# Optimization experiments

Hardware: AMD Instinct MI355X
Metric: run time of the kernel (lower is better)

## Reference

```python
import jax, jax.numpy as jnp
import numpy as np

N_QUERIES = 16384
N_TRAIN = 16384


def setup_inputs() -> dict:
    key = jax.random.key(0)
    k1, k2, k3 = jax.random.split(key, 3)
    queries = jax.random.normal(k1, (N_QUERIES,), dtype=jnp.float32)
    x_train = jax.random.normal(k2, (N_TRAIN,), dtype=jnp.float32)
    y_train = jax.random.normal(k3, (N_TRAIN,), dtype=jnp.float32)
    w = jnp.ones((N_TRAIN,), dtype=jnp.float32)  # learned bandwidth param
    return {"queries": queries, "x_train": x_train, "y_train": y_train, "w": w}


def reference(queries, x_train, y_train, w):
    # pairwise diff: [n_q, n_train]
    diff = queries[:, None] - x_train[None, :]
    scores = -jnp.square(diff * w) * 0.5
    attn = jax.nn.softmax(scores, axis=1)  # [n_q, n_train]
    return attn @ y_train  # [n_q]
```

## Files before the change

### kernel.cpp

```cpp
#include <hip/hip_runtime.h>

#if defined(__has_builtin)
#if __has_builtin(__builtin_amdgcn_exp2f)
#define EXP2F(x) __builtin_amdgcn_exp2f(x)
#endif
#endif
#ifndef EXP2F
#define EXP2F(x) exp2f(x)
#endif

#define BLOCK 256
#define QPT 8
#define TILE 512
#define MAX_SEGS 128
#define RSPLIT 4

typedef float v2f __attribute__((ext_vector_type(2)));

#define KFOLD 0.8493218f

__global__ __launch_bounds__(BLOCK) void nw_partial(
    const float* __restrict__ q, const float* __restrict__ xt,
    const float* __restrict__ yt, const float* __restrict__ w,
    float2* __restrict__ partial, int n_q, int n_t, int segs)
{
    __shared__ float4 tile[TILE];
    const int seg = blockIdx.x;
    const int tid = threadIdx.x;
    const int qbase = blockIdx.y * (BLOCK * QPT) + tid;

    v2f q2[QPT / 2];
    v2f acc[QPT];
#pragma unroll
    for (int i = 0; i < QPT; ++i) {
        int qi = qbase + i * BLOCK;
        float qv = (qi < n_q) ? q[qi] : 0.f;
        if (i & 1) q2[i >> 1].y = qv; else q2[i >> 1].x = qv;
        acc[i] = (v2f){0.f, 0.f};
    }

    const int seg_len = (n_t + segs - 1) / segs;
    const int s0 = seg * seg_len;
    const int s1 = min(s0 + seg_len, n_t);

    for (int base = s0; base < s1; base += TILE) {
        const int cnt = min(TILE, s1 - base);
        __syncthreads();
        for (int j = tid; j < cnt; j += BLOCK) {
            float a = w[base + j] * KFOLD;
            tile[j] = make_float4(a, -xt[base + j] * a, yt[base + j], 0.f);
        }
        __syncthreads();
#pragma unroll 2
        for (int j = 0; j < cnt; ++j) {
            float4 v = tile[j];
            v2f a2  = (v2f){v.x, v.x};
            v2f nb2 = (v2f){v.y, v.y};
            v2f ym  = (v2f){v.z, 1.0f};
#pragma unroll
            for (int p = 0; p < QPT / 2; ++p) {
                v2f t = __builtin_elementwise_fma(q2[p], a2, nb2);
                v2f s = -(t * t);
                float e0 = EXP2F(s.x);
                float e1 = EXP2F(s.y);
                acc[2 * p]     = __builtin_elementwise_fma((v2f){e0, e0}, ym,
                                                           acc[2 * p]);
                acc[2 * p + 1] = __builtin_elementwise_fma((v2f){e1, e1}, ym,
                                                           acc[2 * p + 1]);
            }
        }
    }

#pragma unroll
    for (int i = 0; i < QPT; ++i) {
        int qi = qbase + i * BLOCK;
        if (qi < n_q) partial[seg * n_q + qi] = make_float2(acc[i].x, acc[i].y);
    }
}

__global__ __launch_bounds__(BLOCK) void nw_reduce(
    const float2* __restrict__ partial, float* __restrict__ out,
    int n_q, int segs)
{
    __shared__ float2 red[RSPLIT][64];
    const int tid = threadIdx.x;
    const int c = tid >> 6;
    const int ql = tid & 63;
    const int qi = blockIdx.x * 64 + ql;

    float num = 0.f, den = 0.f;
    if (qi < n_q) {
        for (int s = c; s < segs; s += RSPLIT) {
            float2 p = partial[(size_t)s * n_q + qi];
            num += p.x;
            den += p.y;
        }
    }
    red[c][ql] = make_float2(num, den);
    __syncthreads();
    if (c == 0 && qi < n_q) {
        float2 r1 = red[1][ql], r2 = red[2][ql], r3 = red[3][ql];
        num += r1.x + r2.x + r3.x;
        den += r1.y + r2.y + r3.y;
        out[qi] = num / den;
    }
}

extern "C" void kernel_launch(void* const* d_in, const int* in_sizes, int n_in,
                              void* d_out, int out_size, void* d_ws, size_t ws_size,
                              hipStream_t stream) {
    const float* q  = (const float*)d_in[0];
    const float* xt = (const float*)d_in[1];
    const float* yt = (const float*)d_in[2];
    const float* w  = (const float*)d_in[3];
    const int n_q = in_sizes[0];
    const int n_t = in_sizes[1];

    int segs = MAX_SEGS;
    size_t need = (size_t)segs * (size_t)n_q * sizeof(float2);
    if (need > ws_size) {
        segs = (int)(ws_size / ((size_t)n_q * sizeof(float2)));
        if (segs < 1) segs = 1;
    }

    float2* partial = (float2*)d_ws;
    dim3 grid(segs, (n_q + BLOCK * QPT - 1) / (BLOCK * QPT));
    nw_partial<<<grid, BLOCK, 0, stream>>>(q, xt, yt, w, partial, n_q, n_t, segs);
    nw_reduce<<<(n_q + 63) / 64, BLOCK, 0, stream>>>(partial, (float*)d_out,
                                                     n_q, segs);
}
```

Before: 107.4 us.

## Pair train points per query and accumulate with packed fp16 dot products

Restructures the inner loop so each query processes two training points at once with packed FMAs. The two exponentials are packed to fp16 and accumulated into numerator and denominator with fdot2 against fp16 y values and ones. The shared tile is split into a float4 of scale/bias pairs plus packed half y values, and the segment count doubles to raise parallelism. It aims to cut VALU instructions per pair, but fp16 rounding of the weights and y values loses accuracy, and more segments add reduce traffic.

```diff
diff --git a/kernel.cpp b/kernel.cpp
--- a/kernel.cpp
+++ b/kernel.cpp
@@ -3,6 +3,9 @@
 #if defined(__has_builtin)
 #if __has_builtin(__builtin_amdgcn_exp2f)
 #define EXP2F(x) __builtin_amdgcn_exp2f(x)
+#endif
+#if __has_builtin(__builtin_amdgcn_fdot2)
+#define HAVE_FDOT2 1
 #endif
 #endif
 #ifndef EXP2F
@@ -12,10 +15,12 @@
 #define BLOCK 256
 #define QPT 8
 #define TILE 512
-#define MAX_SEGS 128
+#define TILE2 (TILE / 2)
+#define MAX_SEGS 256
 #define RSPLIT 4
 
 typedef float v2f __attribute__((ext_vector_type(2)));
+typedef _Float16 h2 __attribute__((ext_vector_type(2)));
 
 #define KFOLD 0.8493218f
 
@@ -24,49 +29,74 @@
     const float* __restrict__ yt, const float* __restrict__ w,
     float2* __restrict__ partial, int n_q, int n_t, int segs)
 {
-    __shared__ float4 tile[TILE];
+    __shared__ float4 tileA[TILE2];
+    __shared__ unsigned int tileY[TILE2];
+
     const int seg = blockIdx.x;
     const int tid = threadIdx.x;
     const int qbase = blockIdx.y * (BLOCK * QPT) + tid;
 
-    v2f q2[QPT / 2];
-    v2f acc[QPT];
+    v2f q2[QPT];
+    float num[QPT], den[QPT];
 #pragma unroll
     for (int i = 0; i < QPT; ++i) {
         int qi = qbase + i * BLOCK;
         float qv = (qi < n_q) ? q[qi] : 0.f;
-        if (i & 1) q2[i >> 1].y = qv; else q2[i >> 1].x = qv;
-        acc[i] = (v2f){0.f, 0.f};
+        q2[i] = (v2f){qv, qv};
+        num[i] = 0.f;
+        den[i] = 0.f;
     }
 
     const int seg_len = (n_t + segs - 1) / segs;
     const int s0 = seg * seg_len;
     const int s1 = min(s0 + seg_len, n_t);
 
+    const h2 one2 = {(_Float16)1.0f, (_Float16)1.0f};
+
     for (int base = s0; base < s1; base += TILE) {
         const int cnt = min(TILE, s1 - base);
+        const int cnt2 = (cnt + 1) >> 1;
         __syncthreads();
-        for (int j = tid; j < cnt; j += BLOCK) {
-            float a = w[base + j] * KFOLD;
-            tile[j] = make_float4(a, -xt[base + j] * a, yt[base + j], 0.f);
+        for (int j2 = tid; j2 < cnt2; j2 += BLOCK) {
+            int j0 = base + 2 * j2;
+            int j1 = j0 + 1;
+            float a0 = w[j0] * KFOLD;
+            float nb0 = -xt[j0] * a0;
+            float y0 = yt[j0];
+            float a1 = 0.f, nb1 = 1.0e4f, y1 = 0.f;
+            if (j1 < s1) {
+                a1 = w[j1] * KFOLD;
+                nb1 = -xt[j1] * a1;
+                y1 = yt[j1];
+            }
+            tileA[j2] = make_float4(a0, a1, nb0, nb1);
+            h2 yh = {(_Float16)y0, (_Float16)y1};
+            tileY[j2] = __builtin_bit_cast(unsigned int, yh);
         }
         __syncthreads();
 #pragma unroll 2
-        for (int j = 0; j < cnt; ++j) {
-            float4 v = tile[j];
-            v2f a2  = (v2f){v.x, v.x};
-            v2f nb2 = (v2f){v.y, v.y};
-            v2f ym  = (v2f){v.z, 1.0f};
+        for (int j2 = 0; j2 < cnt2; ++j2) {
+            float4 A = tileA[j2];
+            v2f a2 = (v2f){A.x, A.y};
+            v2f nb2 = (v2f){A.z, A.w};
+            h2 yh = __builtin_bit_cast(h2, tileY[j2]);
+#ifndef HAVE_FDOT2
+            float yf0 = (float)yh.x, yf1 = (float)yh.y;
+#endif
 #pragma unroll
-            for (int p = 0; p < QPT / 2; ++p) {
-                v2f t = __builtin_elementwise_fma(q2[p], a2, nb2);
+            for (int i = 0; i < QPT; ++i) {
+                v2f t = __builtin_elementwise_fma(q2[i], a2, nb2);
                 v2f s = -(t * t);
                 float e0 = EXP2F(s.x);
                 float e1 = EXP2F(s.y);
-                acc[2 * p]     = __builtin_elementwise_fma((v2f){e0, e0}, ym,
-                                                           acc[2 * p]);
-                acc[2 * p + 1] = __builtin_elementwise_fma((v2f){e1, e1}, ym,
-                                                           acc[2 * p + 1]);
+#ifdef HAVE_FDOT2
+                h2 ep = __builtin_bit_cast(h2, __builtin_amdgcn_cvt_pkrtz(e0, e1));
+                num[i] = __builtin_amdgcn_fdot2(ep, yh, num[i], false);
+                den[i] = __builtin_amdgcn_fdot2(ep, one2, den[i], false);
+#else
+                num[i] = fmaf(e0, yf0, fmaf(e1, yf1, num[i]));
+                den[i] += e0 + e1;
+#endif
             }
         }
     }
@@ -74,7 +104,7 @@
 #pragma unroll
     for (int i = 0; i < QPT; ++i) {
         int qi = qbase + i * BLOCK;
-        if (qi < n_q) partial[seg * n_q + qi] = make_float2(acc[i].x, acc[i].y);
+        if (qi < n_q) partial[seg * n_q + qi] = make_float2(num[i], den[i]);
     }
 }
 
```

Result: slower. 122.0 us (+13.6%).
